# Kernel tuning notes

Measured on AMD Instinct MI355X. Metric: run time of the kernel, lower is better.

Reference implementation:

```python
import jax, jax.numpy as jnp
import numpy as np

HEAD_DIM = 64
N_HEADS = 64
N_KV = 8
Q_MULT = N_HEADS // N_KV  # 8
HIDDEN = 2880
SLIDING_WINDOW = 128
BASE = 150000.0
INIT_CTX = 4096
SCALING = 32.0
NTK_ALPHA = 1.0   # beta_slow
NTK_BETA = 32.0   # beta_fast
EPS = 1e-5
SM_SCALE = 1.0 / np.sqrt(HEAD_DIM)


def _cos_sin(num_tokens):
    # YaRN-style NTK rope (scaling_factor > 1 branch)
    freq = BASE ** (jnp.arange(0, HEAD_DIM, 2, dtype=jnp.float32) / HEAD_DIM)
    concentration = 0.1 * np.log(SCALING) + 1.0
    d_half = HEAD_DIM // 2
    low = d_half * np.log(INIT_CTX / (NTK_BETA * 2 * np.pi)) / np.log(BASE)
    high = d_half * np.log(INIT_CTX / (NTK_ALPHA * 2 * np.pi)) / np.log(BASE)
    interpolation = 1.0 / (SCALING * freq)
    extrapolation = 1.0 / freq
    ramp = (jnp.arange(d_half, dtype=jnp.float32) - low) / (high - low)
    mask = 1.0 - jnp.clip(ramp, 0.0, 1.0)
    inv_freq = interpolation * (1.0 - mask) + extrapolation * mask
    t = jnp.arange(num_tokens, dtype=jnp.float32)
    freqs = t[:, None] * inv_freq[None, :]  # [n, d/2]
    return jnp.cos(freqs) * concentration, jnp.sin(freqs) * concentration


def _apply_rotary(x, cos, sin):
    # x: [n, h, d]; cos/sin: [n, d/2]
    cos = cos[:, None, :].astype(x.dtype)
    sin = sin[:, None, :].astype(x.dtype)
    x1, x2 = jnp.split(x, 2, axis=-1)
    return jnp.concatenate((x1 * cos - x2 * sin, x2 * cos + x1 * sin), axis=-1)


def _forward(x, norm_w, qkv_w, out_w, sinks):
    b, s, h = x.shape  # b=1
    n = b * s
    # RMSNorm
    var = jnp.mean(jnp.square(x), axis=-1, keepdims=True)
    t = x * jax.lax.rsqrt(var + EPS) * norm_w
    # QKV projection
    qkv = jnp.einsum('bsh,hf->bsf', t, qkv_w)
    q_dim = N_HEADS * HEAD_DIM
    kv_dim = N_KV * HEAD_DIM
    q = qkv[:, :, :q_dim].reshape(n, N_KV, Q_MULT, HEAD_DIM)
    k = qkv[:, :, q_dim:q_dim + kv_dim].reshape(n, N_KV, HEAD_DIM)
    v = qkv[:, :, q_dim + kv_dim:].reshape(n, N_KV, HEAD_DIM)
    # RoPE
    cos, sin = _cos_sin(n)
    q = _apply_rotary(q.reshape(n, -1, HEAD_DIM), cos, sin).reshape(n, N_KV, Q_MULT, HEAD_DIM)
    k = _apply_rotary(k, cos, sin)
    # sdpa with sliding window + sink logits
    qk = jnp.einsum('qhmd,khd->hmqk', q, k) * SM_SCALE  # [N_KV, Q_MULT, n, n]
    i = jnp.arange(n)[:, None]
    j = jnp.arange(n)[None, :]
    neg_inf = jnp.array(-jnp.inf, dtype=qk.dtype)
    banned = (j > i) | (i - j >= SLIDING_WINDOW)  # causal + sliding window
    qk = jnp.where(banned[None, None, :, :], neg_inf, qk)
    S = jnp.broadcast_to(sinks.reshape(N_KV, Q_MULT, 1, 1), (N_KV, Q_MULT, n, 1))
    logits = jnp.concatenate([qk, S], axis=-1)  # [N_KV, Q_MULT, n, n+1]
    w = jax.nn.softmax(logits, axis=-1)[..., :-1]
    attn = jnp.einsum('hmqk,khd->qhmd', w, v).reshape(n, N_HEADS * HEAD_DIM)
    out = jnp.einsum('qf,fh->qh', attn, out_w)  # [n, hidden]
    return x + out  # broadcasts to [b, s, hidden]


def setup_inputs() -> dict:
    key = jax.random.key(0)
    k1, k2, k3, k4, k5 = jax.random.split(key, 5)
    x = jax.random.normal(k1, (1, 2048, HIDDEN), dtype=jnp.float32)
    norm_w = jax.random.uniform(k2, (HIDDEN,), dtype=jnp.float32, minval=0.5, maxval=1.5)
    qkv_w = jax.random.normal(k3, (HIDDEN, HEAD_DIM * (N_HEADS + 2 * N_KV)), dtype=jnp.float32) * 0.02
    out_w = jax.random.normal(k4, (HEAD_DIM * N_HEADS, HIDDEN), dtype=jnp.float32) * 0.02
    sinks = jax.random.normal(k5, (N_HEADS,), dtype=jnp.float32)
    return {"x": x, "norm_w": norm_w, "qkv_w": qkv_w, "out_w": out_w, "sinks": sinks}


def reference(x, norm_w, qkv_w, out_w, sinks):
    return _forward(x, norm_w, qkv_w, out_w, sinks)
```

## Files before the change

### kernel.cpp

```cpp
#include <hip/hip_runtime.h>
#include <math.h>

typedef unsigned short u16;
typedef unsigned int u32;
typedef short bf4 __attribute__((ext_vector_type(4)));
typedef __bf16 bfv8 __attribute__((ext_vector_type(8)));
typedef float f4 __attribute__((ext_vector_type(4)));

#define SEQ 2048
#define HID 2880
#define KPAD 2944
#define QKVN 5120

static __device__ __forceinline__ u16 f2bf(float x) {
  union { float f; u32 u; } v; v.f = x;
  u32 r = v.u + 0x7fffu + ((v.u >> 16) & 1u);
  return (u16)(r >> 16);
}
static __device__ __forceinline__ float bf2f(u16 s) {
  union { u32 u; float f; } v; v.u = ((u32)s) << 16;
  return v.f;
}
static __device__ __forceinline__ void gl_lds16(const void* g, void* l) {
  __builtin_amdgcn_global_load_lds((const __attribute__((address_space(1))) u32*)g,
                                   (__attribute__((address_space(3))) u32*)l, 16, 0, 0);
}
#define MFMA(a, b, c) __builtin_amdgcn_mfma_f32_16x16x16bf16_1k(a, b, c, 0, 0, 0)
#define MFMA32(a, b, c) __builtin_amdgcn_mfma_f32_16x16x32_bf16(a, b, c, 0, 0, 0)
#define BAR __builtin_amdgcn_s_barrier()
#define SCHEDB __builtin_amdgcn_sched_barrier(0)
#define VMCNT0 asm volatile("s_waitcnt vmcnt(0)" ::: "memory")
#define LGKM0 asm volatile("s_waitcnt lgkmcnt(0)" ::: "memory")

__global__ __launch_bounds__(256) void k_rmsnorm(const float* __restrict__ x,
                                                 const float* __restrict__ w,
                                                 u16* __restrict__ t) {
  const int row = blockIdx.x;
  const float* xr = x + (size_t)row * HID;
  float ss = 0.f;
  for (int i = threadIdx.x; i < 720; i += 256) {
    float4 v = ((const float4*)xr)[i];
    ss += v.x * v.x + v.y * v.y + v.z * v.z + v.w * v.w;
  }
#pragma unroll
  for (int m = 1; m < 64; m <<= 1) ss += __shfl_xor(ss, m);
  __shared__ float red[4];
  if ((threadIdx.x & 63) == 0) red[threadIdx.x >> 6] = ss;
  __syncthreads();
  float sc = rsqrtf((red[0] + red[1] + red[2] + red[3]) * (1.0f / HID) + 1e-5f);
  u16* tr = t + (size_t)row * KPAD;
  for (int i = threadIdx.x; i < 720; i += 256) {
    float4 v = ((const float4*)xr)[i];
    float4 wv = ((const float4*)w)[i];
    ushort4 o;
    o.x = f2bf(v.x * sc * wv.x);
    o.y = f2bf(v.y * sc * wv.y);
    o.z = f2bf(v.z * sc * wv.z);
    o.w = f2bf(v.w * sc * wv.w);
    ((ushort4*)tr)[i] = o;
  }
  if (threadIdx.x < 16) ((ushort4*)tr)[720 + threadIdx.x] = make_ushort4(0, 0, 0, 0);
}

__global__ __launch_bounds__(256) void k_convT(const float* __restrict__ W,
                                               u16* __restrict__ WT, int K, int Kpad,
                                               int Nsrc) {
  __shared__ u16 tile[64][65];
  const int n0 = blockIdx.x * 64, k0 = blockIdx.y * 64;
  for (int s = threadIdx.x; s < 1024; s += 256) {
    int r = s >> 4, c4 = (s & 15) * 4;
    int kk = k0 + r, nn = n0 + c4;
    float4 v = make_float4(0.f, 0.f, 0.f, 0.f);
    if (kk < K && nn < Nsrc) v = *(const float4*)&W[(size_t)kk * Nsrc + nn];
    tile[c4 + 0][r] = f2bf(v.x);
    tile[c4 + 1][r] = f2bf(v.y);
    tile[c4 + 2][r] = f2bf(v.z);
    tile[c4 + 3][r] = f2bf(v.w);
  }
  __syncthreads();
  for (int s = threadIdx.x; s < 512; s += 256) {
    int r = s >> 3, c8 = (s & 7) * 8;
    u32 p0 = tile[r][c8 + 0] | ((u32)tile[r][c8 + 1] << 16);
    u32 p1 = tile[r][c8 + 2] | ((u32)tile[r][c8 + 3] << 16);
    u32 p2 = tile[r][c8 + 4] | ((u32)tile[r][c8 + 5] << 16);
    u32 p3 = tile[r][c8 + 6] | ((u32)tile[r][c8 + 7] << 16);
    *(uint4*)&WT[(size_t)(n0 + r) * Kpad + k0 + c8] = make_uint4(p0, p1, p2, p3);
  }
}

template <int MODE, int BN, int NF1>
__global__ __launch_bounds__(512, 2) void k_gemm2(const u16* __restrict__ A,
                                                  const u16* __restrict__ BT,
                                                  void* __restrict__ Cv,
                                                  const float* __restrict__ resid,
                                                  int N, int Nout, int K) {
  constexpr int WN = BN / 4;
  constexpr int NF = WN / 16;
  constexpr int ABYTES = 128 * 128;
  constexpr int BBYTES = BN * 128;
  constexpr int TILE = ABYTES + BBYTES;
  constexpr int NB = BN / 64;
  __shared__ __align__(16) char lds[2 * TILE];
  const int n0 = blockIdx.x * BN, m0 = blockIdx.y * 128;
  const int tid = threadIdx.x;
  const int l = tid & 63, w = tid >> 6;
  const int wm = w >> 2, wn = w & 3;
  const int g = l >> 4, q = l & 15;
  const int NT = K >> 6;
  const int srow = tid >> 3;
  const int sc8 = ((tid & 7) ^ (srow & 7)) * 8;

#define STAGE_A(bo, kt, qa) gl_lds16(A + (size_t)(m0 + (qa)*64 + srow) * K + (kt)*64 + sc8, \
    lds + (bo) + (qa)*8192 + tid*16)
#define STAGE_B(bo, kt, qb) gl_lds16(BT + (size_t)(n0 + (qb)*64 + srow) * K + (kt)*64 + sc8, \
    lds + (bo) + ABYTES + (qb)*8192 + tid*16)

  f4 acc[4][NF] = {};
#pragma unroll
  for (int qa = 0; qa < 2; ++qa) STAGE_A(0, 0, qa);
#pragma unroll
  for (int qb = 0; qb < NB; ++qb) STAGE_B(0, 0, qb);
  VMCNT0; SCHEDB; BAR;

  for (int t = 0; t < NT; ++t) {
    const int bo = (t & 1) * TILE;
    const int so = bo ^ TILE;
    bfv8 af[4][2], bfr[NF][2];
    if (t + 1 < NT) {
#pragma unroll
      for (int qa = 0; qa < 2; ++qa) STAGE_A(so, t + 1, qa);
#pragma unroll
      for (int qb = 0; qb < NB; ++qb) STAGE_B(so, t + 1, qb);
    }
#pragma unroll
    for (int mf = 0; mf < 4; ++mf) {
      const int r = wm * 64 + mf * 16 + q;
#pragma unroll
      for (int ks = 0; ks < 2; ++ks)
        af[mf][ks] = *(const bfv8*)(lds + bo + r * 128 + (((ks * 4 + g) ^ (r & 7)) << 4));
    }
#pragma unroll
    for (int nf = 0; nf < NF1; ++nf) {
      const int r = wn * WN + nf * 16 + q;
#pragma unroll
      for (int ks = 0; ks < 2; ++ks)
        bfr[nf][ks] = *(const bfv8*)(lds + bo + ABYTES + r * 128 + (((ks * 4 + g) ^ (r & 7)) << 4));
    }
    LGKM0; SCHEDB;
    __builtin_amdgcn_s_setprio(1);
#pragma unroll
    for (int mf = 0; mf < 4; ++mf)
#pragma unroll
      for (int nf = 0; nf < NF1; ++nf) {
        acc[mf][nf] = MFMA32(af[mf][0], bfr[nf][0], acc[mf][nf]);
        acc[mf][nf] = MFMA32(af[mf][1], bfr[nf][1], acc[mf][nf]);
      }
    __builtin_amdgcn_s_setprio(0);
    SCHEDB; BAR;
#pragma unroll
    for (int nf = NF1; nf < NF; ++nf) {
      const int r = wn * WN + nf * 16 + q;
#pragma unroll
      for (int ks = 0; ks < 2; ++ks)
        bfr[nf][ks] = *(const bfv8*)(lds + bo + ABYTES + r * 128 + (((ks * 4 + g) ^ (r & 7)) << 4));
    }
    LGKM0; SCHEDB;
    __builtin_amdgcn_s_setprio(1);
#pragma unroll
    for (int mf = 0; mf < 4; ++mf)
#pragma unroll
      for (int nf = NF1; nf < NF; ++nf) {
        acc[mf][nf] = MFMA32(af[mf][0], bfr[nf][0], acc[mf][nf]);
        acc[mf][nf] = MFMA32(af[mf][1], bfr[nf][1], acc[mf][nf]);
      }
    __builtin_amdgcn_s_setprio(0);
    VMCNT0;
    SCHEDB; BAR;
  }
#pragma unroll
  for (int mf = 0; mf < 4; ++mf)
#pragma unroll
    for (int nf = 0; nf < NF; ++nf)
#pragma unroll
      for (int r = 0; r < 4; ++r) {
        int row = m0 + wm * 64 + mf * 16 + g * 4 + r;
        int col = n0 + wn * WN + nf * 16 + q;
        if constexpr (MODE == 0) {
          ((u16*)Cv)[(size_t)row * N + col] = f2bf(acc[mf][nf][r]);
        } else {
          if (col < Nout)
            ((float*)Cv)[(size_t)row * Nout + col] =
                acc[mf][nf][r] + resid[(size_t)row * Nout + col];
        }
      }
#undef STAGE_A
#undef STAGE_B
}

__global__ __launch_bounds__(256) void k_rope(u16* __restrict__ qkv) {
  const int t = blockIdx.y;
  const int i = blockIdx.x * 256 + threadIdx.x;
  const int d = i & 31, hd = i >> 5;
  const float low = 8.0927791f, high = 17.3980236f, conc = 1.3465735903f;
  float freq = powf(150000.0f, (float)d * (1.0f / 32.0f));
  float r01 = fminf(fmaxf(((float)d - low) / (high - low), 0.f), 1.f);
  float invf = (1.0f / (32.0f * freq)) * r01 + (1.0f / freq) * (1.f - r01);
  float ang = (float)t * invf;
  float cc = cosf(ang) * conc;
  float ss = sinf(ang) * conc;
  u16* base = qkv + (size_t)t * QKVN + (hd < 64 ? hd * 64 : 4096 + (hd - 64) * 64);
  float x1 = bf2f(base[d]), x2 = bf2f(base[d + 32]);
  base[d] = f2bf(x1 * cc - x2 * ss);
  base[d + 32] = f2bf(x2 * cc + x1 * ss);
}

__global__ __launch_bounds__(256) void k_vtrans(const u16* __restrict__ qkv,
                                                u16* __restrict__ vt) {
  __shared__ u16 tile[64][72];
  const int t0 = blockIdx.x * 64, h = blockIdx.y;
  for (int s = threadIdx.x; s < 512; s += 256) {
    int r = s >> 3, c8 = (s & 7) * 8;
    uint4 v = *(const uint4*)&qkv[(size_t)(t0 + r) * QKVN + 4608 + h * 64 + c8];
    *(uint4*)&tile[r][c8] = v;
  }
  __syncthreads();
  for (int s = threadIdx.x; s < 512; s += 256) {
    int d = s >> 3, c8 = (s & 7) * 8;
    u32 p0 = tile[c8 + 0][d] | ((u32)tile[c8 + 1][d] << 16);
    u32 p1 = tile[c8 + 2][d] | ((u32)tile[c8 + 3][d] << 16);
    u32 p2 = tile[c8 + 4][d] | ((u32)tile[c8 + 5][d] << 16);
    u32 p3 = tile[c8 + 6][d] | ((u32)tile[c8 + 7][d] << 16);
    *(uint4*)&vt[((size_t)h * 64 + d) * SEQ + t0 + c8] = make_uint4(p0, p1, p2, p3);
  }
}

__global__ __launch_bounds__(512) void k_attn(const u16* __restrict__ qkv,
                                              const u16* __restrict__ vt,
                                              const float* __restrict__ sinks,
                                              u16* __restrict__ attn) {
  __shared__ u16 lK[144 * 72];
  __shared__ u16 lV[64 * 152];
  __shared__ u16 lP[8 * 16 * 148];
  const int t0 = blockIdx.x * 16;
  const int h = blockIdx.y;
  const int j0 = t0 - 128;
  const int tid = threadIdx.x;
  for (int s = tid; s < 1152; s += 512) {
    int row = s >> 3, c = s & 7;
    int j = j0 + row;
    uint4 v = make_uint4(0, 0, 0, 0);
    if (j >= 0) v = *(const uint4*)&qkv[(size_t)j * QKVN + 4096 + h * 64 + c * 8];
    *(uint4*)&lK[row * 72 + c * 8] = v;
  }
  for (int s = tid; s < 1152; s += 512) {
    int d = s / 18, c = s - d * 18;
    int jb = j0 + c * 8;
    uint4 v = make_uint4(0, 0, 0, 0);
    if (jb >= 0) v = *(const uint4*)&vt[((size_t)h * 64 + d) * SEQ + jb];
    *(uint4*)&lV[d * 152 + c * 8] = v;
  }
  __syncthreads();
  const int w = tid >> 6, l = tid & 63;
  const int g = l >> 4, q = l & 15;
  const int hq = h * 8 + w;
  const float sink = sinks[hq];
  bf4 qf[4];
  const u16* qrow = qkv + (size_t)(t0 + q) * QKVN + hq * 64;
#pragma unroll
  for (int ks = 0; ks < 4; ++ks) qf[ks] = *(const bf4*)&qrow[ks * 16 + g * 4];
  f4 sacc[9];
#pragma unroll
  for (int nt = 0; nt < 9; ++nt) {
    f4 z = {0.f, 0.f, 0.f, 0.f};
    sacc[nt] = z;
#pragma unroll
    for (int ks = 0; ks < 4; ++ks) {
      bf4 kf = *(const bf4*)&lK[(nt * 16 + q) * 72 + ks * 16 + g * 4];
      sacc[nt] = MFMA(qf[ks], kf, sacc[nt]);
    }
  }
  const float NEG = -__builtin_inff();
  float rmax[4] = {NEG, NEG, NEG, NEG};
#pragma unroll
  for (int nt = 0; nt < 9; ++nt)
#pragma unroll
    for (int r = 0; r < 4; ++r) {
      float sv = sacc[nt][r] * 0.125f;
      int it = t0 + g * 4 + r;
      int j = j0 + nt * 16 + q;
      bool ban = (j > it) || (it - j >= 128) || (j < 0);
      sv = ban ? NEG : sv;
      sacc[nt][r] = sv;
      rmax[r] = fmaxf(rmax[r], sv);
    }
#pragma unroll
  for (int r = 0; r < 4; ++r)
#pragma unroll
    for (int m = 1; m < 16; m <<= 1) rmax[r] = fmaxf(rmax[r], __shfl_xor(rmax[r], m));
  float ssum[4];
  u16* pbase = lP + w * (16 * 148);
#pragma unroll
  for (int r = 0; r < 4; ++r) {
    float mf = fmaxf(rmax[r], sink);
    float ps = 0.f;
#pragma unroll
    for (int nt = 0; nt < 9; ++nt) {
      float p = __expf(sacc[nt][r] - mf);
      pbase[(g * 4 + r) * 148 + nt * 16 + q] = f2bf(p);
      ps += p;
    }
#pragma unroll
    for (int m = 1; m < 16; m <<= 1) ps += __shfl_xor(ps, m);
    ssum[r] = ps + __expf(sink - mf);
  }
  f4 oacc[4] = {};
#pragma unroll
  for (int kt = 0; kt < 9; ++kt) {
    bf4 pa = *(const bf4*)&pbase[q * 148 + kt * 16 + g * 4];
#pragma unroll
    for (int nt = 0; nt < 4; ++nt) {
      bf4 vf = *(const bf4*)&lV[(nt * 16 + q) * 152 + kt * 16 + g * 4];
      oacc[nt] = MFMA(pa, vf, oacc[nt]);
    }
  }
#pragma unroll
  for (int nt = 0; nt < 4; ++nt)
#pragma unroll
    for (int r = 0; r < 4; ++r) {
      int row = t0 + g * 4 + r;
      attn[(size_t)row * 4096 + hq * 64 + nt * 16 + q] = f2bf(oacc[nt][r] / ssum[r]);
    }
}

extern "C" void kernel_launch(void* const* d_in, const int* in_sizes, int n_in,
                              void* d_out, int out_size, void* d_ws, size_t ws_size,
                              hipStream_t stream) {
  const float* x = (const float*)d_in[0];
  const float* norm_w = (const float*)d_in[1];
  const float* qkv_w = (const float*)d_in[2];
  const float* out_w = (const float*)d_in[3];
  const float* sinks = (const float*)d_in[4];
  float* out = (float*)d_out;
  char* ws = (char*)d_ws;
  u16* t     = (u16*)(ws);
  u16* wqkvT = (u16*)(ws + 12058624);
  u16* qkv   = (u16*)(ws + 42205184);
  u16* vt    = (u16*)(ws + 63176704);
  u16* woutT = (u16*)(ws + 65273856);
  u16* attnO = (u16*)(ws);

  k_rmsnorm<<<dim3(2048), dim3(256), 0, stream>>>(x, norm_w, t);
  k_convT<<<dim3(80, 46), dim3(256), 0, stream>>>(qkv_w, wqkvT, 2880, KPAD, 5120);
  k_convT<<<dim3(48, 64), dim3(256), 0, stream>>>(out_w, woutT, 4096, 4096, 2880);
  k_gemm2<0, 320, 3><<<dim3(16, 16), dim3(512), 0, stream>>>(t, wqkvT, (void*)qkv,
                                                             nullptr, 5120, 5120, KPAD);
  k_rope<<<dim3(9, 2048), dim3(256), 0, stream>>>(qkv);
  k_vtrans<<<dim3(32, 8), dim3(256), 0, stream>>>(qkv, vt);
  k_attn<<<dim3(128, 8), dim3(512), 0, stream>>>(qkv, vt, sinks, attnO);
  k_gemm2<1, 192, 2><<<dim3(16, 16), dim3(512), 0, stream>>>(attnO, woutT, (void*)out,
                                                             x, 3072, 2880, 4096);
}
```

Measured before the change: 213.1 us.

## Pipeline B-fragment LDS loads across MFMA columns and share RoPE cos/sin per token

The GEMM inner loop now keeps a two-deep ring of B fragments. It waits on partial lgkmcnt so each column's MFMAs can start while the next fragment's LDS read is still in flight, and it drops the mid-tile barrier and the two-phase split. This is meant to hide LDS latency and cut register use for B fragments, but relies on precise waitcnt counting. Separately, RoPE launches one block per token, computes cos/sin once into shared memory and loops over heads. That removes the redundant transcendental work each thread did before.

```diff
diff --git a/kernel.cpp b/kernel.cpp
--- a/kernel.cpp
+++ b/kernel.cpp
@@ -31,6 +31,7 @@
 #define SCHEDB __builtin_amdgcn_sched_barrier(0)
 #define VMCNT0 asm volatile("s_waitcnt vmcnt(0)" ::: "memory")
 #define LGKM0 asm volatile("s_waitcnt lgkmcnt(0)" ::: "memory")
+#define LGKM2 asm volatile("s_waitcnt lgkmcnt(2)" ::: "memory")
 
 __global__ __launch_bounds__(256) void k_rmsnorm(const float* __restrict__ x,
                                                  const float* __restrict__ w,
@@ -88,17 +89,17 @@
   }
 }
 
-template <int MODE, int BN, int NF1>
-__global__ __launch_bounds__(512, 2) void k_gemm2(const u16* __restrict__ A,
+template <int MODE, int BN>
+__global__ __launch_bounds__(512, 2) void k_gemm3(const u16* __restrict__ A,
                                                   const u16* __restrict__ BT,
                                                   void* __restrict__ Cv,
                                                   const float* __restrict__ resid,
                                                   int N, int Nout, int K) {
   constexpr int WN = BN / 4;
   constexpr int NF = WN / 16;
-  constexpr int ABYTES = 128 * 128;
-  constexpr int BBYTES = BN * 128;
-  constexpr int TILE = ABYTES + BBYTES;
+  constexpr int ABY = 128 * 128;
+  constexpr int BBY = BN * 128;
+  constexpr int TILE = ABY + BBY;
   constexpr int NB = BN / 64;
   __shared__ __align__(16) char lds[2 * TILE];
   const int n0 = blockIdx.x * BN, m0 = blockIdx.y * 128;
@@ -113,7 +114,10 @@
 #define STAGE_A(bo, kt, qa) gl_lds16(A + (size_t)(m0 + (qa)*64 + srow) * K + (kt)*64 + sc8, \
     lds + (bo) + (qa)*8192 + tid*16)
 #define STAGE_B(bo, kt, qb) gl_lds16(BT + (size_t)(n0 + (qb)*64 + srow) * K + (kt)*64 + sc8, \
-    lds + (bo) + ABYTES + (qb)*8192 + tid*16)
+    lds + (bo) + ABY + (qb)*8192 + tid*16)
+#define LDB2(dst, nf) { const int r = wn * WN + (nf)*16 + q; \
+    dst[0] = *(const bfv8*)(lds + bo + ABY + r * 128 + (((g) ^ (r & 7)) << 4)); \
+    dst[1] = *(const bfv8*)(lds + bo + ABY + r * 128 + (((4 + g) ^ (r & 7)) << 4)); }
 
   f4 acc[4][NF] = {};
 #pragma unroll
@@ -125,54 +129,35 @@
   for (int t = 0; t < NT; ++t) {
     const int bo = (t & 1) * TILE;
     const int so = bo ^ TILE;
-    bfv8 af[4][2], bfr[NF][2];
     if (t + 1 < NT) {
 #pragma unroll
       for (int qa = 0; qa < 2; ++qa) STAGE_A(so, t + 1, qa);
 #pragma unroll
       for (int qb = 0; qb < NB; ++qb) STAGE_B(so, t + 1, qb);
     }
+    SCHEDB;
+    bfv8 af[4][2], bb[2][2];
 #pragma unroll
     for (int mf = 0; mf < 4; ++mf) {
       const int r = wm * 64 + mf * 16 + q;
-#pragma unroll
-      for (int ks = 0; ks < 2; ++ks)
-        af[mf][ks] = *(const bfv8*)(lds + bo + r * 128 + (((ks * 4 + g) ^ (r & 7)) << 4));
-    }
-#pragma unroll
-    for (int nf = 0; nf < NF1; ++nf) {
-      const int r = wn * WN + nf * 16 + q;
-#pragma unroll
-      for (int ks = 0; ks < 2; ++ks)
-        bfr[nf][ks] = *(const bfv8*)(lds + bo + ABYTES + r * 128 + (((ks * 4 + g) ^ (r & 7)) << 4));
-    }
-    LGKM0; SCHEDB;
+      af[mf][0] = *(const bfv8*)(lds + bo + r * 128 + (((g) ^ (r & 7)) << 4));
+      af[mf][1] = *(const bfv8*)(lds + bo + r * 128 + (((4 + g) ^ (r & 7)) << 4));
+    }
+    LDB2(bb[0], 0);
+    SCHEDB;
+    LDB2(bb[1], 1);
     __builtin_amdgcn_s_setprio(1);
 #pragma unroll
-    for (int mf = 0; mf < 4; ++mf)
-#pragma unroll
-      for (int nf = 0; nf < NF1; ++nf) {
-        acc[mf][nf] = MFMA32(af[mf][0], bfr[nf][0], acc[mf][nf]);
-        acc[mf][nf] = MFMA32(af[mf][1], bfr[nf][1], acc[mf][nf]);
+    for (int nf = 0; nf < NF; ++nf) {
+      if (nf == NF - 1) { LGKM0; } else { LGKM2; }
+      SCHEDB;
+#pragma unroll
+      for (int mf = 0; mf < 4; ++mf) {
+        acc[mf][nf] = MFMA32(af[mf][0], bb[nf & 1][0], acc[mf][nf]);
+        acc[mf][nf] = MFMA32(af[mf][1], bb[nf & 1][1], acc[mf][nf]);
       }
-    __builtin_amdgcn_s_setprio(0);
-    SCHEDB; BAR;
-#pragma unroll
-    for (int nf = NF1; nf < NF; ++nf) {
-      const int r = wn * WN + nf * 16 + q;
-#pragma unroll
-      for (int ks = 0; ks < 2; ++ks)
-        bfr[nf][ks] = *(const bfv8*)(lds + bo + ABYTES + r * 128 + (((ks * 4 + g) ^ (r & 7)) << 4));
-    }
-    LGKM0; SCHEDB;
-    __builtin_amdgcn_s_setprio(1);
-#pragma unroll
-    for (int mf = 0; mf < 4; ++mf)
-#pragma unroll
-      for (int nf = NF1; nf < NF; ++nf) {
-        acc[mf][nf] = MFMA32(af[mf][0], bfr[nf][0], acc[mf][nf]);
-        acc[mf][nf] = MFMA32(af[mf][1], bfr[nf][1], acc[mf][nf]);
-      }
+      if (nf + 2 < NF) LDB2(bb[nf & 1], nf + 2);
+    }
     __builtin_amdgcn_s_setprio(0);
     VMCNT0;
     SCHEDB; BAR;
@@ -195,23 +180,31 @@
       }
 #undef STAGE_A
 #undef STAGE_B
+#undef LDB2
 }
 
 __global__ __launch_bounds__(256) void k_rope(u16* __restrict__ qkv) {
-  const int t = blockIdx.y;
-  const int i = blockIdx.x * 256 + threadIdx.x;
-  const int d = i & 31, hd = i >> 5;
-  const float low = 8.0927791f, high = 17.3980236f, conc = 1.3465735903f;
-  float freq = powf(150000.0f, (float)d * (1.0f / 32.0f));
-  float r01 = fminf(fmaxf(((float)d - low) / (high - low), 0.f), 1.f);
-  float invf = (1.0f / (32.0f * freq)) * r01 + (1.0f / freq) * (1.f - r01);
-  float ang = (float)t * invf;
-  float cc = cosf(ang) * conc;
-  float ss = sinf(ang) * conc;
-  u16* base = qkv + (size_t)t * QKVN + (hd < 64 ? hd * 64 : 4096 + (hd - 64) * 64);
-  float x1 = bf2f(base[d]), x2 = bf2f(base[d + 32]);
-  base[d] = f2bf(x1 * cc - x2 * ss);
-  base[d + 32] = f2bf(x2 * cc + x1 * ss);
+  __shared__ float lcs[64];
+  const int t = blockIdx.x;
+  if (threadIdx.x < 32) {
+    const int d = threadIdx.x;
+    const float low = 8.0927791f, high = 17.3980236f, conc = 1.3465735903f;
+    float freq = powf(150000.0f, (float)d * (1.0f / 32.0f));
+    float r01 = fminf(fmaxf(((float)d - low) / (high - low), 0.f), 1.f);
+    float invf = (1.0f / (32.0f * freq)) * r01 + (1.0f / freq) * (1.f - r01);
+    float ang = (float)t * invf;
+    lcs[d] = cosf(ang) * conc;
+    lcs[d + 32] = sinf(ang) * conc;
+  }
+  __syncthreads();
+  for (int i = threadIdx.x; i < 2304; i += 256) {
+    const int d = i & 31, hd = i >> 5;
+    u16* base = qkv + (size_t)t * QKVN + (hd < 64 ? hd * 64 : 4096 + (hd - 64) * 64);
+    float cc = lcs[d], ss = lcs[d + 32];
+    float x1 = bf2f(base[d]), x2 = bf2f(base[d + 32]);
+    base[d] = f2bf(x1 * cc - x2 * ss);
+    base[d + 32] = f2bf(x2 * cc + x1 * ss);
+  }
 }
 
 __global__ __launch_bounds__(256) void k_vtrans(const u16* __restrict__ qkv,
@@ -352,11 +345,11 @@
   k_rmsnorm<<<dim3(2048), dim3(256), 0, stream>>>(x, norm_w, t);
   k_convT<<<dim3(80, 46), dim3(256), 0, stream>>>(qkv_w, wqkvT, 2880, KPAD, 5120);
   k_convT<<<dim3(48, 64), dim3(256), 0, stream>>>(out_w, woutT, 4096, 4096, 2880);
-  k_gemm2<0, 320, 3><<<dim3(16, 16), dim3(512), 0, stream>>>(t, wqkvT, (void*)qkv,
-                                                             nullptr, 5120, 5120, KPAD);
-  k_rope<<<dim3(9, 2048), dim3(256), 0, stream>>>(qkv);
+  k_gemm3<0, 320><<<dim3(16, 16), dim3(512), 0, stream>>>(t, wqkvT, (void*)qkv,
+                                                          nullptr, 5120, 5120, KPAD);
+  k_rope<<<dim3(2048), dim3(256), 0, stream>>>(qkv);
   k_vtrans<<<dim3(32, 8), dim3(256), 0, stream>>>(qkv, vt);
   k_attn<<<dim3(128, 8), dim3(512), 0, stream>>>(qkv, vt, sinks, attnO);
-  k_gemm2<1, 192, 2><<<dim3(16, 16), dim3(512), 0, stream>>>(attnO, woutT, (void*)out,
-                                                             x, 3072, 2880, 4096);
-}
+  k_gemm3<1, 192><<<dim3(16, 16), dim3(512), 0, stream>>>(attnO, woutT, (void*)out,
+                                                          x, 3072, 2880, 4096);
+}
```

Result: faster. 185.2 us (-13.1%).
